# Kernel optimization log

Hardware: AMD Instinct MI355X
Metric: run time of the kernel (lower is better)

## Reference

```python
import jax, jax.numpy as jnp
import numpy as np
import math

# Module hyperparameters (match init_kwargs)
B_CAPS = 16   # input capsule types
C_CAPS = 32   # output capsule types
KSZ = 3       # kernel size
STRIDE = 1
P = 4         # pose matrix is P x P
PSIZE = P * P
LAMBDA = 0.01 # EM routing inverse-temperature (argv[1])
EPS = 1e-6
LN_2PI = math.log(2.0 * math.pi)


def patching(x, K, stride):
    """(b,h,w,B,d) -> (b,oh,ow,K*K*B,d), im2col-style window gather."""
    b, h, w, Bc, d = x.shape
    oh = (h - K) // stride + 1
    idxs = np.array([[hi + k for k in range(K)] for hi in range(0, h - K + 1, stride)])  # (oh, K)
    x = x[:, idxs]                                  # (b, oh, K, w, Bc, d)
    x = x[:, :, :, idxs]                            # (b, oh, K, ow, K, Bc, d)
    x = jnp.transpose(x, (0, 1, 3, 2, 4, 5, 6))     # (b, oh, ow, K, K, Bc, d)
    return x.reshape(b, oh, oh, K * K * Bc, d), oh, oh


def em_routing(v, a_in, beta_u, beta_a, lam, iters):
    """EM routing (Hinton et al., Matrix Capsules with EM Routing).
    v: (b,h,w,N,C,psize) votes; a_in: (b,h,w,N,1) input activations.
    Returns mu (b,h,w,C,psize), a_out (b,h,w,C,1).
    """
    b, h, w, N, C, ps = v.shape
    # r: assignment of input capsule i to output capsule j, weighted by a_in
    r = jnp.full((b, h, w, N, C), 1.0 / C, dtype=v.dtype) * a_in  # (b,h,w,N,C)
    for it in range(iters):
        # ---- M step ----
        r_sum = r.sum(axis=3, keepdims=True)                   # (b,h,w,1,C)
        coeff = (r / (r_sum + EPS))[..., None]                 # (b,h,w,N,C,1)
        mu = jnp.sum(coeff * v, axis=3, keepdims=True)         # (b,h,w,1,C,ps)
        sigma_sq = jnp.sum(coeff * (v - mu) ** 2, axis=3, keepdims=True) + EPS
        # beta_u: (C,1) broadcasts over the psize axis
        cost_h = (beta_u + 0.5 * jnp.log(sigma_sq)) * r_sum[..., None]  # (b,h,w,1,C,ps)
        logit = lam * (beta_a - cost_h.sum(axis=5, keepdims=True))      # (b,h,w,1,C,1)
        a_out = jax.nn.sigmoid(logit)
        # ---- E step ----
        if it < iters - 1:
            ln_p = (-((v - mu) ** 2) / (2.0 * sigma_sq)
                    - 0.5 * jnp.log(sigma_sq) - 0.5 * LN_2PI)   # (b,h,w,N,C,ps)
            ln_ap = ln_p.sum(axis=5) + jnp.log(a_out[..., 0] + EPS)  # (b,h,w,N,C)
            r = jax.nn.softmax(ln_ap, axis=4) * a_in
    mu = mu.reshape(b, h, w, C, ps)
    a_out = a_out.reshape(b, h, w, C, 1)
    return mu, a_out


def setup_inputs() -> dict:
    key = jax.random.key(0)
    k1, k2, k3 = jax.random.split(key, 3)
    x = jax.random.normal(k1, (4, 16, 16, B_CAPS, PSIZE), dtype=jnp.float32)
    a = jax.random.uniform(k2, (4, 16, 16, B_CAPS, 1), dtype=jnp.float32)
    weight = jax.random.normal(k3, (1, 1, 1, KSZ * KSZ * B_CAPS, C_CAPS, P, P), dtype=jnp.float32)
    beta_u = jnp.zeros((C_CAPS, 1), dtype=jnp.float32)
    beta_a = jnp.zeros((C_CAPS, 1), dtype=jnp.float32)
    return {"x": x, "a": a, "weight": weight, "beta_u": beta_u, "beta_a": beta_a, "iters": 2}


def reference(x, a, weight, beta_u, beta_a, iters):
    b = x.shape[0]
    p_in, oh, ow = patching(x, KSZ, STRIDE)   # (b,oh,ow,K*K*B,psize)
    a_in, _, _ = patching(a, KSZ, STRIDE)     # (b,oh,ow,K*K*B,1)
    N = KSZ * KSZ * B_CAPS
    # voting: per-capsule pose matmul x(P,P) @ W(P,P) broadcast over C
    v = jnp.einsum('bhwnij,ncjk->bhwncik',
                   p_in.reshape(b, oh, ow, N, P, P),
                   weight.reshape(N, C_CAPS, P, P))
    v = v.reshape(b, oh, ow, N, C_CAPS, PSIZE)
    p_out, a_out = em_routing(v, a_in, beta_u, beta_a, LAMBDA, iters)
    return p_out, a_out
```

## Files before the change

kernel.cpp:

```cpp
#include <hip/hip_runtime.h>


namespace {

constexpr int OHW  = 14;
constexpr int NPOS = 4 * OHW * OHW;
constexpr int NN   = 144;
constexpr int CC   = 32;
constexpr float LAMB  = 0.01f;
constexpr float EPSF  = 1e-6f;
constexpr float LN2PI = 1.8378770664093453f;
constexpr int RS = 33;

__device__ __forceinline__ void mat44(const float4 pr[4], const float4 wr[4], float v[16]) {
  #pragma unroll
  for (int i = 0; i < 4; ++i) {
    v[4*i+0] = fmaf(pr[i].x, wr[0].x, fmaf(pr[i].y, wr[1].x, fmaf(pr[i].z, wr[2].x, pr[i].w * wr[3].x)));
    v[4*i+1] = fmaf(pr[i].x, wr[0].y, fmaf(pr[i].y, wr[1].y, fmaf(pr[i].z, wr[2].y, pr[i].w * wr[3].y)));
    v[4*i+2] = fmaf(pr[i].x, wr[0].z, fmaf(pr[i].y, wr[1].z, fmaf(pr[i].z, wr[2].z, pr[i].w * wr[3].z)));
    v[4*i+3] = fmaf(pr[i].x, wr[0].w, fmaf(pr[i].y, wr[1].w, fmaf(pr[i].z, wr[2].w, pr[i].w * wr[3].w)));
  }
}

__global__ __launch_bounds__(256)
void convcaps_em(const float* __restrict__ x,
                 const float* __restrict__ a,
                 const float* __restrict__ w,
                 const float* __restrict__ beta_u,
                 const float* __restrict__ beta_a,
                 const int*   __restrict__ iters_p,
                 float* __restrict__ out_mu,
                 float* __restrict__ out_a)
{
  __shared__ __align__(16) float sP[NN * 16];
  __shared__ float sA[NN];
  __shared__ float sR[NN * RS];

  const int tid = threadIdx.x;
  const int pos = blockIdx.x;
  const int b   = pos / (OHW * OHW);
  const int rem = pos - b * (OHW * OHW);
  const int oi  = rem / OHW;
  const int oj  = rem - oi * OHW;

  int iters = iters_p[0];
  iters = (iters < 1) ? 1 : (iters > 16 ? 16 : iters);

  #pragma unroll
  for (int t = 0; t < 9; ++t) {
    const int kh = t / 3, kw = t % 3;
    sP[t * 256 + tid] = x[(((b * 16 + oi + kh) * 16) + (oj + kw)) * 256 + tid];
  }
  if (tid < NN) {
    const int kh = tid / 48, kw = (tid >> 4) % 3, bc = tid & 15;
    sA[tid] = a[(((b * 16 + oi + kh) * 16) + (oj + kw)) * 16 + bc];
  }
  __syncthreads();
  #pragma unroll
  for (int t = 0; t < 18; ++t) {
    const int idx = t * 256 + tid;
    const int n = idx >> 5, c = idx & 31;
    sR[n * RS + c] = sA[n] * (1.0f / CC);
  }
  __syncthreads();

  const int lane = tid & 63;
  const int wv   = tid >> 6;
  const int c    = wv * 8 + (lane & 7);
  const int sub  = lane >> 3;
  const float bu = beta_u[c];
  const float ba = beta_a[c];

  float mu[16], hi[16];

  for (int it = 0; it < iters; ++it) {
    float rs = 0.f;
    #pragma unroll
    for (int k = 0; k < 18; ++k) rs += sR[(sub + 8 * k) * RS + c];
    rs += __shfl_xor(rs, 8);
    rs += __shfl_xor(rs, 16);
    rs += __shfl_xor(rs, 32);
    const float inv = 1.0f / (rs + EPSF);

    float S0 = 0.f, S1[16], S2[16];
    #pragma unroll
    for (int p = 0; p < 16; ++p) { S1[p] = 0.f; S2[p] = 0.f; }

    for (int k = 0; k < 18; ++k) {
      const int n = sub + 8 * k;
      const float coeff = sR[n * RS + c] * inv;
      const float4* Pp = (const float4*)(sP + n * 16);
      const float4 pr[4] = {Pp[0], Pp[1], Pp[2], Pp[3]};
      const float4* Wp = (const float4*)(w + n * 512 + c * 16);
      const float4 wr[4] = {Wp[0], Wp[1], Wp[2], Wp[3]};
      float v[16];
      mat44(pr, wr, v);
      S0 += coeff;
      #pragma unroll
      for (int p = 0; p < 16; ++p) {
        S1[p] = fmaf(coeff, v[p], S1[p]);
        S2[p] = fmaf(coeff * v[p], v[p], S2[p]);
      }
    }
    #pragma unroll
    for (int m = 8; m <= 32; m <<= 1) {
      S0 += __shfl_xor(S0, m);
      #pragma unroll
      for (int p = 0; p < 16; ++p) {
        S1[p] += __shfl_xor(S1[p], m);
        S2[p] += __shfl_xor(S2[p], m);
      }
    }

    float logsum = 0.f;
    #pragma unroll
    for (int p = 0; p < 16; ++p) {
      mu[p] = S1[p];
      float sig = S2[p] - mu[p] * (2.0f * S1[p] - mu[p] * S0) + EPSF;
      sig = fmaxf(sig, 1e-12f);
      logsum += __logf(sig);
      hi[p] = 0.5f / sig;
    }
    const float cost = rs * (16.0f * bu + 0.5f * logsum);
    const float aout = 1.0f / (1.0f + __expf(-LAMB * (ba - cost)));

    if (it == iters - 1) {
      if (sub == 0) {
        float4* om = (float4*)(out_mu + (size_t)pos * 512 + c * 16);
        om[0] = make_float4(mu[0],  mu[1],  mu[2],  mu[3]);
        om[1] = make_float4(mu[4],  mu[5],  mu[6],  mu[7]);
        om[2] = make_float4(mu[8],  mu[9],  mu[10], mu[11]);
        om[3] = make_float4(mu[12], mu[13], mu[14], mu[15]);
        out_a[pos * CC + c] = aout;
      }
    } else {
      const float kc = __logf(aout + EPSF) - 0.5f * logsum - 8.0f * LN2PI;
      for (int k = 0; k < 18; ++k) {
        const int n = sub + 8 * k;
        const float4* Pp = (const float4*)(sP + n * 16);
        const float4 pr[4] = {Pp[0], Pp[1], Pp[2], Pp[3]};
        const float4* Wp = (const float4*)(w + n * 512 + c * 16);
        const float4 wr[4] = {Wp[0], Wp[1], Wp[2], Wp[3]};
        float v[16];
        mat44(pr, wr, v);
        float s = 0.f;
        #pragma unroll
        for (int p = 0; p < 16; ++p) {
          const float d = v[p] - mu[p];
          s = fmaf(d * d, hi[p], s);
        }
        sR[n * RS + c] = kc - s;
      }
      __syncthreads();
      if (tid < NN) {
        float xv[32];
        float mx = -3.0e38f;
        #pragma unroll
        for (int q = 0; q < 32; ++q) { xv[q] = sR[tid * RS + q]; mx = fmaxf(mx, xv[q]); }
        float ssum = 0.f;
        #pragma unroll
        for (int q = 0; q < 32; ++q) { xv[q] = __expf(xv[q] - mx); ssum += xv[q]; }
        const float sc = sA[tid] / ssum;
        #pragma unroll
        for (int q = 0; q < 32; ++q) sR[tid * RS + q] = xv[q] * sc;
      }
      __syncthreads();
    }
  }
}

}

extern "C" void kernel_launch(void* const* d_in, const int* in_sizes, int n_in,
                              void* d_out, int out_size, void* d_ws, size_t ws_size,
                              hipStream_t stream) {
  const float* x  = (const float*)d_in[0];
  const float* a  = (const float*)d_in[1];
  const float* w  = (const float*)d_in[2];
  const float* bu = (const float*)d_in[3];
  const float* ba = (const float*)d_in[4];
  const int* iters = (const int*)d_in[5];

  float* out_mu = (float*)d_out;
  float* out_a  = out_mu + (size_t)NPOS * CC * 16;

  convcaps_em<<<NPOS, 256, 0, stream>>>(x, a, w, bu, ba, iters, out_mu, out_a);
}
```

Measured before the change: 124.9 us.

## Fuse E-step softmax into M-step accumulation, dropping the shared routing matrix

Removes the NN x 32 shared routing matrix. The first M-step uses uniform assignments derived directly from the input activations. Later iterations compute each vote once and apply an in-register softmax over output capsules, using shuffles within 8 lanes plus a small double-buffered cross-wave exchange, then accumulate the weighted moments immediately. This avoids recomputing the votes between the E and M steps, the serial 144-thread softmax pass and most shared-memory traffic, but adds one block barrier per chunk and extra exp work. The pose rows are padded to a stride of 20 and the next weight load is prefetched.

```diff
diff --git a/kernel.cpp b/kernel.cpp
--- a/kernel.cpp
+++ b/kernel.cpp
@@ -10,7 +10,7 @@
 constexpr float LAMB  = 0.01f;
 constexpr float EPSF  = 1e-6f;
 constexpr float LN2PI = 1.8378770664093453f;
-constexpr int RS = 33;
+constexpr int PSTR = 20;
 
 __device__ __forceinline__ void mat44(const float4 pr[4], const float4 wr[4], float v[16]) {
   #pragma unroll
@@ -32,9 +32,9 @@
                  float* __restrict__ out_mu,
                  float* __restrict__ out_a)
 {
-  __shared__ __align__(16) float sP[NN * 16];
-  __shared__ float sA[NN];
-  __shared__ float sR[NN * RS];
+  __shared__ __align__(16) float sP[NN * PSTR];
+  __shared__ float  sA[NN];
+  __shared__ float2 sMB[2][4][8];
 
   const int tid = threadIdx.x;
   const int pos = blockIdx.x;
@@ -49,18 +49,13 @@
   #pragma unroll
   for (int t = 0; t < 9; ++t) {
     const int kh = t / 3, kw = t % 3;
-    sP[t * 256 + tid] = x[(((b * 16 + oi + kh) * 16) + (oj + kw)) * 256 + tid];
+    const int idx = t * 256 + tid;
+    const float val = x[(((b * 16 + oi + kh) * 16) + (oj + kw)) * 256 + tid];
+    sP[(idx >> 4) * PSTR + (idx & 15)] = val;
   }
   if (tid < NN) {
     const int kh = tid / 48, kw = (tid >> 4) % 3, bc = tid & 15;
     sA[tid] = a[(((b * 16 + oi + kh) * 16) + (oj + kw)) * 16 + bc];
-  }
-  __syncthreads();
-  #pragma unroll
-  for (int t = 0; t < 18; ++t) {
-    const int idx = t * 256 + tid;
-    const int n = idx >> 5, c = idx & 31;
-    sR[n * RS + c] = sA[n] * (1.0f / CC);
   }
   __syncthreads();
 
@@ -68,104 +63,147 @@
   const int wv   = tid >> 6;
   const int c    = wv * 8 + (lane & 7);
   const int sub  = lane >> 3;
-  const float bu = beta_u[c];
-  const float ba = beta_a[c];
+  const float bu16 = 16.0f * beta_u[c];
+  const float ba   = beta_a[c];
+
+  float rs = 0.f;
+  #pragma unroll
+  for (int k = 0; k < 18; ++k) rs += sA[sub + 8 * k];
+  rs += __shfl_xor(rs, 8);
+  rs += __shfl_xor(rs, 16);
+  rs += __shfl_xor(rs, 32);
+  rs *= (1.0f / CC);
+  const float cw = 1.0f / (CC * (rs + EPSF));
+
+  float S0 = 0.f, S1[16], S2[16];
+  #pragma unroll
+  for (int p = 0; p < 16; ++p) { S1[p] = 0.f; S2[p] = 0.f; }
+
+  for (int k = 0; k < 18; ++k) {
+    const int n = sub + 8 * k;
+    const float4* Pp = (const float4*)(sP + n * PSTR);
+    const float4 pr[4] = {Pp[0], Pp[1], Pp[2], Pp[3]};
+    const float4* Wp = (const float4*)(w + n * 512 + c * 16);
+    const float4 wr[4] = {Wp[0], Wp[1], Wp[2], Wp[3]};
+    float v[16];
+    mat44(pr, wr, v);
+    const float coeff = sA[n] * cw;
+    S0 += coeff;
+    #pragma unroll
+    for (int p = 0; p < 16; ++p) {
+      S1[p] = fmaf(coeff, v[p], S1[p]);
+      S2[p] = fmaf(coeff * v[p], v[p], S2[p]);
+    }
+  }
+  #pragma unroll
+  for (int m = 8; m <= 32; m <<= 1) {
+    S0 += __shfl_xor(S0, m);
+    #pragma unroll
+    for (int p = 0; p < 16; ++p) {
+      S1[p] += __shfl_xor(S1[p], m);
+      S2[p] += __shfl_xor(S2[p], m);
+    }
+  }
 
   float mu[16], hi[16];
-
-  for (int it = 0; it < iters; ++it) {
-    float rs = 0.f;
-    #pragma unroll
-    for (int k = 0; k < 18; ++k) rs += sR[(sub + 8 * k) * RS + c];
-    rs += __shfl_xor(rs, 8);
-    rs += __shfl_xor(rs, 16);
-    rs += __shfl_xor(rs, 32);
-    const float inv = 1.0f / (rs + EPSF);
-
-    float S0 = 0.f, S1[16], S2[16];
-    #pragma unroll
-    for (int p = 0; p < 16; ++p) { S1[p] = 0.f; S2[p] = 0.f; }
-
-    for (int k = 0; k < 18; ++k) {
-      const int n = sub + 8 * k;
-      const float coeff = sR[n * RS + c] * inv;
-      const float4* Pp = (const float4*)(sP + n * 16);
+  float logsum = 0.f;
+  #pragma unroll
+  for (int p = 0; p < 16; ++p) {
+    mu[p] = S1[p];
+    float sig = S2[p] - mu[p] * (2.0f * S1[p] - mu[p] * S0) + EPSF;
+    sig = fmaxf(sig, 1e-12f);
+    logsum += __logf(sig);
+    hi[p] = 0.5f / sig;
+  }
+  float cost = rs * (bu16 + 0.5f * logsum);
+  float aout = 1.0f / (1.0f + __expf(-LAMB * (ba - cost)));
+
+  for (int it = 1; it < iters; ++it) {
+    const float kc = __logf(aout + EPSF) - 0.5f * logsum - 8.0f * LN2PI;
+    float T0 = 0.f, T1[16], T2[16];
+    #pragma unroll
+    for (int p = 0; p < 16; ++p) { T1[p] = 0.f; T2[p] = 0.f; }
+
+    const float4* W0 = (const float4*)(w + sub * 512 + c * 16);
+    float4 wr[4] = {W0[0], W0[1], W0[2], W0[3]};
+
+    #pragma unroll 1
+    for (int ch = 0; ch < 18; ++ch) {
+      const int n = sub + 8 * ch;
+      const float4* Pp = (const float4*)(sP + n * PSTR);
       const float4 pr[4] = {Pp[0], Pp[1], Pp[2], Pp[3]};
-      const float4* Wp = (const float4*)(w + n * 512 + c * 16);
-      const float4 wr[4] = {Wp[0], Wp[1], Wp[2], Wp[3]};
       float v[16];
       mat44(pr, wr, v);
-      S0 += coeff;
+      if (ch < 17) {
+        const float4* Wn = (const float4*)(w + (n + 8) * 512 + c * 16);
+        wr[0] = Wn[0]; wr[1] = Wn[1]; wr[2] = Wn[2]; wr[3] = Wn[3];
+      }
+      float s = 0.f;
       #pragma unroll
       for (int p = 0; p < 16; ++p) {
-        S1[p] = fmaf(coeff, v[p], S1[p]);
-        S2[p] = fmaf(coeff * v[p], v[p], S2[p]);
-      }
-    }
-    #pragma unroll
-    for (int m = 8; m <= 32; m <<= 1) {
-      S0 += __shfl_xor(S0, m);
+        const float d = v[p] - mu[p];
+        s = fmaf(d * d, hi[p], s);
+      }
+      const float xv = kc - s;
+      float m8 = xv;
+      m8 = fmaxf(m8, __shfl_xor(m8, 1));
+      m8 = fmaxf(m8, __shfl_xor(m8, 2));
+      m8 = fmaxf(m8, __shfl_xor(m8, 4));
+      const float e = __expf(xv - m8);
+      float z8 = e;
+      z8 += __shfl_xor(z8, 1);
+      z8 += __shfl_xor(z8, 2);
+      z8 += __shfl_xor(z8, 4);
+      const int par = (it * 18 + ch) & 1;
+      if ((lane & 7) == 0) sMB[par][wv][sub] = make_float2(m8, z8);
+      __syncthreads();
+      const float2 q0 = sMB[par][0][sub];
+      const float2 q1 = sMB[par][1][sub];
+      const float2 q2 = sMB[par][2][sub];
+      const float2 q3 = sMB[par][3][sub];
+      const float M = fmaxf(fmaxf(q0.x, q1.x), fmaxf(q2.x, q3.x));
+      const float Z = fmaf(q0.y, __expf(q0.x - M),
+                      fmaf(q1.y, __expf(q1.x - M),
+                      fmaf(q2.y, __expf(q2.x - M),
+                           q3.y * __expf(q3.x - M))));
+      const float rn = sA[n] * e * __expf(m8 - M) * __builtin_amdgcn_rcpf(Z);
+      T0 += rn;
       #pragma unroll
       for (int p = 0; p < 16; ++p) {
-        S1[p] += __shfl_xor(S1[p], m);
-        S2[p] += __shfl_xor(S2[p], m);
-      }
-    }
-
-    float logsum = 0.f;
+        T1[p] = fmaf(rn, v[p], T1[p]);
+        T2[p] = fmaf(rn * v[p], v[p], T2[p]);
+      }
+    }
+    #pragma unroll
+    for (int m = 8; m <= 32; m <<= 1) {
+      T0 += __shfl_xor(T0, m);
+      #pragma unroll
+      for (int p = 0; p < 16; ++p) {
+        T1[p] += __shfl_xor(T1[p], m);
+        T2[p] += __shfl_xor(T2[p], m);
+      }
+    }
+    const float inv1 = 1.0f / (T0 + EPSF);
+    logsum = 0.f;
     #pragma unroll
     for (int p = 0; p < 16; ++p) {
-      mu[p] = S1[p];
-      float sig = S2[p] - mu[p] * (2.0f * S1[p] - mu[p] * S0) + EPSF;
+      mu[p] = T1[p] * inv1;
+      float sig = fmaf(mu[p], fmaf(mu[p], T0, -2.0f * T1[p]), T2[p]) * inv1 + EPSF;
       sig = fmaxf(sig, 1e-12f);
       logsum += __logf(sig);
       hi[p] = 0.5f / sig;
     }
-    const float cost = rs * (16.0f * bu + 0.5f * logsum);
-    const float aout = 1.0f / (1.0f + __expf(-LAMB * (ba - cost)));
-
-    if (it == iters - 1) {
-      if (sub == 0) {
-        float4* om = (float4*)(out_mu + (size_t)pos * 512 + c * 16);
-        om[0] = make_float4(mu[0],  mu[1],  mu[2],  mu[3]);
-        om[1] = make_float4(mu[4],  mu[5],  mu[6],  mu[7]);
-        om[2] = make_float4(mu[8],  mu[9],  mu[10], mu[11]);
-        om[3] = make_float4(mu[12], mu[13], mu[14], mu[15]);
-        out_a[pos * CC + c] = aout;
-      }
-    } else {
-      const float kc = __logf(aout + EPSF) - 0.5f * logsum - 8.0f * LN2PI;
-      for (int k = 0; k < 18; ++k) {
-        const int n = sub + 8 * k;
-        const float4* Pp = (const float4*)(sP + n * 16);
-        const float4 pr[4] = {Pp[0], Pp[1], Pp[2], Pp[3]};
-        const float4* Wp = (const float4*)(w + n * 512 + c * 16);
-        const float4 wr[4] = {Wp[0], Wp[1], Wp[2], Wp[3]};
-        float v[16];
-        mat44(pr, wr, v);
-        float s = 0.f;
-        #pragma unroll
-        for (int p = 0; p < 16; ++p) {
-          const float d = v[p] - mu[p];
-          s = fmaf(d * d, hi[p], s);
-        }
-        sR[n * RS + c] = kc - s;
-      }
-      __syncthreads();
-      if (tid < NN) {
-        float xv[32];
-        float mx = -3.0e38f;
-        #pragma unroll
-        for (int q = 0; q < 32; ++q) { xv[q] = sR[tid * RS + q]; mx = fmaxf(mx, xv[q]); }
-        float ssum = 0.f;
-        #pragma unroll
-        for (int q = 0; q < 32; ++q) { xv[q] = __expf(xv[q] - mx); ssum += xv[q]; }
-        const float sc = sA[tid] / ssum;
-        #pragma unroll
-        for (int q = 0; q < 32; ++q) sR[tid * RS + q] = xv[q] * sc;
-      }
-      __syncthreads();
-    }
+    cost = T0 * (bu16 + 0.5f * logsum);
+    aout = 1.0f / (1.0f + __expf(-LAMB * (ba - cost)));
+  }
+
+  if (sub == 0) {
+    float4* om = (float4*)(out_mu + (size_t)pos * 512 + c * 16);
+    om[0] = make_float4(mu[0],  mu[1],  mu[2],  mu[3]);
+    om[1] = make_float4(mu[4],  mu[5],  mu[6],  mu[7]);
+    om[2] = make_float4(mu[8],  mu[9],  mu[10], mu[11]);
+    om[3] = make_float4(mu[12], mu[13], mu[14], mu[15]);
+    out_a[pos * CC + c] = aout;
   }
 }
 
```

Result: no change. 123.4 us (-1.1%).

## Fuse E-step softmax into M-step accumulation with lane-per-capsule layout

Applied to the files above, without the earlier changes.

Remaps threads so each lane owns one output capsule and 8 sub-groups split the input capsules. The E-step log-likelihood and the softmax over output capsules (via wave shuffles) are now computed inline while accumulating the next M-step statistics. This removes the stored routing matrix in shared memory and one extra recomputation pass of votes per iteration. Partial sums are reduced across waves through shared memory instead of long shuffle chains. Weights are software-prefetched one step ahead, at the cost of more registers.

```diff
diff --git a/kernel.cpp b/kernel.cpp
--- a/kernel.cpp
+++ b/kernel.cpp
@@ -10,7 +10,9 @@
 constexpr float LAMB  = 0.01f;
 constexpr float EPSF  = 1e-6f;
 constexpr float LN2PI = 1.8378770664093453f;
-constexpr int RS = 33;
+constexpr int NSUB = 8;
+constexpr int NCH  = NN / NSUB;
+constexpr int RST  = 36;
 
 __device__ __forceinline__ void mat44(const float4 pr[4], const float4 wr[4], float v[16]) {
   #pragma unroll
@@ -34,7 +36,8 @@
 {
   __shared__ __align__(16) float sP[NN * 16];
   __shared__ float sA[NN];
-  __shared__ float sR[NN * RS];
+  __shared__ __align__(16) float sRed[4][CC][RST];
+  __shared__ __align__(16) float sStat[CC][RST];
 
   const int tid = threadIdx.x;
   const int pos = blockIdx.x;
@@ -56,116 +59,170 @@
     sA[tid] = a[(((b * 16 + oi + kh) * 16) + (oj + kw)) * 16 + bc];
   }
   __syncthreads();
-  #pragma unroll
-  for (int t = 0; t < 18; ++t) {
-    const int idx = t * 256 + tid;
-    const int n = idx >> 5, c = idx & 31;
-    sR[n * RS + c] = sA[n] * (1.0f / CC);
-  }
-  __syncthreads();
 
   const int lane = tid & 63;
   const int wv   = tid >> 6;
-  const int c    = wv * 8 + (lane & 7);
-  const int sub  = lane >> 3;
-  const float bu = beta_u[c];
-  const float ba = beta_a[c];
-
-  float mu[16], hi[16];
+  const int c    = lane & 31;
+  const int half = lane >> 5;
+  const int sub  = wv * 2 + half;
+  const float bu16 = 16.0f * beta_u[c];
+  const float ba   = beta_a[c];
+
+  float mu[16], hi[16], hm[16];
+  float kcp = 0.f, aout = 0.f;
 
   for (int it = 0; it < iters; ++it) {
-    float rs = 0.f;
+    float T0 = 0.f, T1[16], T2[16];
     #pragma unroll
-    for (int k = 0; k < 18; ++k) rs += sR[(sub + 8 * k) * RS + c];
-    rs += __shfl_xor(rs, 8);
-    rs += __shfl_xor(rs, 16);
-    rs += __shfl_xor(rs, 32);
-    const float inv = 1.0f / (rs + EPSF);
-
-    float S0 = 0.f, S1[16], S2[16];
+    for (int p = 0; p < 16; ++p) { T1[p] = 0.f; T2[p] = 0.f; }
+
+    const float4* W0 = (const float4*)(w + sub * 512 + c * 16);
+    float4 wr[4] = {W0[0], W0[1], W0[2], W0[3]};
+
+    if (it == 0) {
+      #pragma unroll 1
+      for (int ch = 0; ch < NCH; ++ch) {
+        const int n = sub + NSUB * ch;
+        const float4* Pp = (const float4*)(sP + n * 16);
+        const float4 pr[4] = {Pp[0], Pp[1], Pp[2], Pp[3]};
+        float v[16];
+        mat44(pr, wr, v);
+        if (ch < NCH - 1) {
+          const float4* Wn = (const float4*)(w + (n + NSUB) * 512 + c * 16);
+          wr[0] = Wn[0]; wr[1] = Wn[1]; wr[2] = Wn[2]; wr[3] = Wn[3];
+        }
+        const float rn = sA[n];
+        T0 += rn;
+        #pragma unroll
+        for (int p = 0; p < 16; ++p) {
+          const float rv = rn * v[p];
+          T1[p] += rv;
+          T2[p] = fmaf(rv, v[p], T2[p]);
+        }
+      }
+    } else {
+      #pragma unroll 1
+      for (int ch = 0; ch < NCH; ++ch) {
+        const int n = sub + NSUB * ch;
+        const float4* Pp = (const float4*)(sP + n * 16);
+        const float4 pr[4] = {Pp[0], Pp[1], Pp[2], Pp[3]};
+        float v[16];
+        mat44(pr, wr, v);
+        if (ch < NCH - 1) {
+          const float4* Wn = (const float4*)(w + (n + NSUB) * 512 + c * 16);
+          wr[0] = Wn[0]; wr[1] = Wn[1]; wr[2] = Wn[2]; wr[3] = Wn[3];
+        }
+        float s0 = 0.f, s1 = 0.f, s2 = 0.f, s3 = 0.f;
+        #pragma unroll
+        for (int p = 0; p < 4; ++p) {
+          s0 = fmaf(fmaf(hi[p],      v[p],      hm[p]),      v[p],      s0);
+          s1 = fmaf(fmaf(hi[p + 4],  v[p + 4],  hm[p + 4]),  v[p + 4],  s1);
+          s2 = fmaf(fmaf(hi[p + 8],  v[p + 8],  hm[p + 8]),  v[p + 8],  s2);
+          s3 = fmaf(fmaf(hi[p + 12], v[p + 12], hm[p + 12]), v[p + 12], s3);
+        }
+        const float xv = kcp - ((s0 + s1) + (s2 + s3));
+        float m = xv;
+        m = fmaxf(m, __shfl_xor(m, 1));
+        m = fmaxf(m, __shfl_xor(m, 2));
+        m = fmaxf(m, __shfl_xor(m, 4));
+        m = fmaxf(m, __shfl_xor(m, 8));
+        m = fmaxf(m, __shfl_xor(m, 16));
+        const float e = __expf(xv - m);
+        float z = e;
+        z += __shfl_xor(z, 1);
+        z += __shfl_xor(z, 2);
+        z += __shfl_xor(z, 4);
+        z += __shfl_xor(z, 8);
+        z += __shfl_xor(z, 16);
+        const float rn = sA[n] * e * __builtin_amdgcn_rcpf(z);
+        T0 += rn;
+        #pragma unroll
+        for (int p = 0; p < 16; ++p) {
+          const float rv = rn * v[p];
+          T1[p] += rv;
+          T2[p] = fmaf(rv, v[p], T2[p]);
+        }
+      }
+    }
+
+    T0 += __shfl_xor(T0, 32);
     #pragma unroll
-    for (int p = 0; p < 16; ++p) { S1[p] = 0.f; S2[p] = 0.f; }
-
-    for (int k = 0; k < 18; ++k) {
-      const int n = sub + 8 * k;
-      const float coeff = sR[n * RS + c] * inv;
-      const float4* Pp = (const float4*)(sP + n * 16);
-      const float4 pr[4] = {Pp[0], Pp[1], Pp[2], Pp[3]};
-      const float4* Wp = (const float4*)(w + n * 512 + c * 16);
-      const float4 wr[4] = {Wp[0], Wp[1], Wp[2], Wp[3]};
-      float v[16];
-      mat44(pr, wr, v);
-      S0 += coeff;
-      #pragma unroll
-      for (int p = 0; p < 16; ++p) {
-        S1[p] = fmaf(coeff, v[p], S1[p]);
-        S2[p] = fmaf(coeff * v[p], v[p], S2[p]);
-      }
-    }
-    #pragma unroll
-    for (int m = 8; m <= 32; m <<= 1) {
-      S0 += __shfl_xor(S0, m);
-      #pragma unroll
-      for (int p = 0; p < 16; ++p) {
-        S1[p] += __shfl_xor(S1[p], m);
-        S2[p] += __shfl_xor(S2[p], m);
-      }
-    }
-
+    for (int p = 0; p < 16; ++p) {
+      T1[p] += __shfl_xor(T1[p], 32);
+      T2[p] += __shfl_xor(T2[p], 32);
+    }
+
+    if (half == 0) {
+      float4* d = (float4*)(&sRed[wv][c][0]);
+      d[0] = make_float4(T1[0],  T1[1],  T1[2],  T1[3]);
+      d[1] = make_float4(T1[4],  T1[5],  T1[6],  T1[7]);
+      d[2] = make_float4(T1[8],  T1[9],  T1[10], T1[11]);
+      d[3] = make_float4(T1[12], T1[13], T1[14], T1[15]);
+      d[4] = make_float4(T2[0],  T2[1],  T2[2],  T2[3]);
+      d[5] = make_float4(T2[4],  T2[5],  T2[6],  T2[7]);
+      d[6] = make_float4(T2[8],  T2[9],  T2[10], T2[11]);
+      d[7] = make_float4(T2[12], T2[13], T2[14], T2[15]);
+      sRed[wv][c][32] = T0;
+    }
+    __syncthreads();
+    {
+      const int c2 = tid & 31;
+      const int s2 = tid >> 5;
+      const float q0 = sRed[0][c2][s2]      + sRed[1][c2][s2]      + sRed[2][c2][s2]      + sRed[3][c2][s2];
+      const float q1 = sRed[0][c2][s2 + 8]  + sRed[1][c2][s2 + 8]  + sRed[2][c2][s2 + 8]  + sRed[3][c2][s2 + 8];
+      const float q2 = sRed[0][c2][s2 + 16] + sRed[1][c2][s2 + 16] + sRed[2][c2][s2 + 16] + sRed[3][c2][s2 + 16];
+      const float q3 = sRed[0][c2][s2 + 24] + sRed[1][c2][s2 + 24] + sRed[2][c2][s2 + 24] + sRed[3][c2][s2 + 24];
+      sStat[c2][s2]      = q0;
+      sStat[c2][s2 + 8]  = q1;
+      sStat[c2][s2 + 16] = q2;
+      sStat[c2][s2 + 24] = q3;
+      if (tid < 32)
+        sStat[tid][32] = sRed[0][tid][32] + sRed[1][tid][32] + sRed[2][tid][32] + sRed[3][tid][32];
+    }
+    __syncthreads();
+
+    const float4* R = (const float4*)(&sStat[c][0]);
+    const float4 u1a = R[0], u1b = R[1], u1c = R[2], u1d = R[3];
+    const float4 u2a = R[4], u2b = R[5], u2c = R[6], u2d = R[7];
+    const float U0 = sStat[c][32];
+    float U1[16] = {u1a.x,u1a.y,u1a.z,u1a.w, u1b.x,u1b.y,u1b.z,u1b.w,
+                    u1c.x,u1c.y,u1c.z,u1c.w, u1d.x,u1d.y,u1d.z,u1d.w};
+    float U2[16] = {u2a.x,u2a.y,u2a.z,u2a.w, u2b.x,u2b.y,u2b.z,u2b.w,
+                    u2c.x,u2c.y,u2c.z,u2c.w, u2d.x,u2d.y,u2d.z,u2d.w};
+
+    const float inv  = 1.0f / (U0 + ((it == 0) ? (CC * EPSF) : EPSF));
+    const float rsum = (it == 0) ? U0 * (1.0f / CC) : U0;
     float logsum = 0.f;
     #pragma unroll
     for (int p = 0; p < 16; ++p) {
-      mu[p] = S1[p];
-      float sig = S2[p] - mu[p] * (2.0f * S1[p] - mu[p] * S0) + EPSF;
+      const float m = U1[p] * inv;
+      mu[p] = m;
+      float sig = fmaf(m, fmaf(m, U0, -2.0f * U1[p]), U2[p]) * inv + EPSF;
       sig = fmaxf(sig, 1e-12f);
       logsum += __logf(sig);
       hi[p] = 0.5f / sig;
     }
-    const float cost = rs * (16.0f * bu + 0.5f * logsum);
-    const float aout = 1.0f / (1.0f + __expf(-LAMB * (ba - cost)));
-
-    if (it == iters - 1) {
-      if (sub == 0) {
-        float4* om = (float4*)(out_mu + (size_t)pos * 512 + c * 16);
-        om[0] = make_float4(mu[0],  mu[1],  mu[2],  mu[3]);
-        om[1] = make_float4(mu[4],  mu[5],  mu[6],  mu[7]);
-        om[2] = make_float4(mu[8],  mu[9],  mu[10], mu[11]);
-        om[3] = make_float4(mu[12], mu[13], mu[14], mu[15]);
-        out_a[pos * CC + c] = aout;
+    const float cost = rsum * (bu16 + 0.5f * logsum);
+    aout = 1.0f / (1.0f + __expf(-LAMB * (ba - cost)));
+
+    if (it < iters - 1) {
+      float K = 0.f;
+      #pragma unroll
+      for (int p = 0; p < 16; ++p) {
+        hm[p] = -2.0f * hi[p] * mu[p];
+        K = fmaf(hi[p] * mu[p], mu[p], K);
       }
-    } else {
-      const float kc = __logf(aout + EPSF) - 0.5f * logsum - 8.0f * LN2PI;
-      for (int k = 0; k < 18; ++k) {
-        const int n = sub + 8 * k;
-        const float4* Pp = (const float4*)(sP + n * 16);
-        const float4 pr[4] = {Pp[0], Pp[1], Pp[2], Pp[3]};
-        const float4* Wp = (const float4*)(w + n * 512 + c * 16);
-        const float4 wr[4] = {Wp[0], Wp[1], Wp[2], Wp[3]};
-        float v[16];
-        mat44(pr, wr, v);
-        float s = 0.f;
-        #pragma unroll
-        for (int p = 0; p < 16; ++p) {
-          const float d = v[p] - mu[p];
-          s = fmaf(d * d, hi[p], s);
-        }
-        sR[n * RS + c] = kc - s;
-      }
-      __syncthreads();
-      if (tid < NN) {
-        float xv[32];
-        float mx = -3.0e38f;
-        #pragma unroll
-        for (int q = 0; q < 32; ++q) { xv[q] = sR[tid * RS + q]; mx = fmaxf(mx, xv[q]); }
-        float ssum = 0.f;
-        #pragma unroll
-        for (int q = 0; q < 32; ++q) { xv[q] = __expf(xv[q] - mx); ssum += xv[q]; }
-        const float sc = sA[tid] / ssum;
-        #pragma unroll
-        for (int q = 0; q < 32; ++q) sR[tid * RS + q] = xv[q] * sc;
-      }
-      __syncthreads();
-    }
+      kcp = __logf(aout + EPSF) - 0.5f * logsum - 8.0f * LN2PI - K;
+    }
+  }
+
+  if (tid < 32) {
+    float4* om = (float4*)(out_mu + (size_t)pos * 512 + c * 16);
+    om[0] = make_float4(mu[0],  mu[1],  mu[2],  mu[3]);
+    om[1] = make_float4(mu[4],  mu[5],  mu[6],  mu[7]);
+    om[2] = make_float4(mu[8],  mu[9],  mu[10], mu[11]);
+    om[3] = make_float4(mu[12], mu[13], mu[14], mu[15]);
+    out_a[pos * CC + c] = aout;
   }
 }
 
```

New measurement: 121.9 us. 1.02x faster.
